# Kernel tuning notes

Measured on AMD Instinct MI355X. Metric: run time of the kernel, lower is better.

## Reference

```python
import jax, jax.numpy as jnp
import numpy as np

B, T, C = 8, 512, 1024
H, E = 16, 64          # n_head, head_dim; H*E == C
L = 2048               # cached (prefix) length in the KV cache


def setup_inputs() -> dict:
    key = jax.random.key(0)
    ks = jax.random.split(key, 6)
    scale = 0.02
    return {
        "x": jax.random.normal(ks[0], (B, T, C), jnp.float32),
        "k_cache": jax.random.normal(ks[1], (B, H, L, E), jnp.float32),
        "v_cache": jax.random.normal(ks[2], (B, H, L, E), jnp.float32),
        "Wqkv": jax.random.normal(ks[3], (C, 3 * C), jnp.float32) * scale,
        "bqkv": jnp.zeros((3 * C,), jnp.float32),
        "Wproj": jax.random.normal(ks[4], (C, C), jnp.float32) * scale,
        "bproj": jnp.zeros((C,), jnp.float32),
    }


def reference(x, k_cache, v_cache, Wqkv, bqkv, Wproj, bproj):
    qkv = x @ Wqkv + bqkv
    q, k, v = jnp.split(qkv, 3, axis=-1)

    def to_heads(t):
        return t.reshape(B, T, H, E).transpose(0, 2, 1, 3)

    q, k, v = to_heads(q), to_heads(k), to_heads(v)

    # append new k,v to the cache (kv_cache.update + get)
    k_full = jnp.concatenate([k_cache, k], axis=2)  # (B,H,L+T,E)
    v_full = jnp.concatenate([v_cache, v], axis=2)

    # manual self-attention with cache-offset causal mask: row i (global pos L+i)
    # may attend to cols j <= L+i  (bias[L:L+T, :L+T])
    att = jnp.einsum("bhte,bhse->bhts", q, k_full) * (1.0 / np.sqrt(E))
    i = jnp.arange(T)[:, None] + L
    j = jnp.arange(L + T)[None, :]
    att = jnp.where(j <= i, att, -jnp.inf)
    att = jax.nn.softmax(att, axis=-1)

    y = jnp.einsum("bhts,bhse->bhte", att, v_full)
    y = y.transpose(0, 2, 1, 3).reshape(B, T, C)
    return y @ Wproj + bproj
```

## Files before the change

### kernel.cpp

```cpp
#include <hip/hip_runtime.h>
#include <hip/hip_bf16.h>

typedef unsigned short u16;
typedef unsigned int u32;

constexpr int B_ = 8, T_ = 512, C_ = 1024, H_ = 16, E_ = 64, L_ = 2048;
constexpr int S_ = L_ + T_;

typedef __bf16 bf16x8 __attribute__((ext_vector_type(8)));
typedef float f32x4 __attribute__((ext_vector_type(4)));
typedef float f32x16 __attribute__((ext_vector_type(16)));

#define QSCALE 0.18033688011112042f


__device__ inline u16 f2bf(float f) {
  u32 u = __float_as_uint(f);
  u32 r = (u + 0x7fffu + ((u >> 16) & 1u)) >> 16;
  return (u16)r;
}

__device__ inline u32 pk2(float a, float b) {
  u32 r;
  asm("v_cvt_pk_bf16_f32 %0, %1, %2" : "=v"(r) : "v"(a), "v"(b));
  return r;
}

__device__ inline void pl32swap(u32& a, u32& b) {
  asm("v_permlane32_swap_b32 %0, %1" : "+v"(a), "+v"(b));
}

__device__ inline void gload_lds16(const u16* g, u16* l) {
  __builtin_amdgcn_global_load_lds(
      (const __attribute__((address_space(1))) u32*)g,
      (__attribute__((address_space(3))) u32*)l, 16, 0, 0);
}

__global__ __launch_bounds__(256) void convert_f32_bf16(const float* __restrict__ in,
                                                        u16* __restrict__ out) {
  const int i = blockIdx.x * 256 + threadIdx.x;
  const float4 a0 = ((const float4*)in)[i * 2];
  const float4 a1 = ((const float4*)in)[i * 2 + 1];
  uint4 p;
  p.x = pk2(a0.x, a0.y);
  p.y = pk2(a0.z, a0.w);
  p.z = pk2(a1.x, a1.y);
  p.w = pk2(a1.z, a1.w);
  ((uint4*)out)[i] = p;
}

__global__ __launch_bounds__(256) void transpose_f32_bf16(const float* __restrict__ in,
                                                          u16* __restrict__ out,
                                                          int R, int Ccols) {
  __shared__ u16 tile[64][65];
  const int r0 = blockIdx.y * 64;
  const int c0 = blockIdx.x * 64;
  const int tr = threadIdx.x >> 6;
  const int tc = threadIdx.x & 63;
#pragma unroll
  for (int i = 0; i < 16; ++i)
    tile[tr + i * 4][tc] = f2bf(in[(size_t)(r0 + tr + i * 4) * Ccols + c0 + tc]);
  __syncthreads();
#pragma unroll
  for (int i = 0; i < 16; ++i)
    out[(size_t)(c0 + tr + i * 4) * R + r0 + tc] = tile[tc][tr + i * 4];
}

__global__ __launch_bounds__(256) void prep_kv(const float* __restrict__ kc,
                                               const float* __restrict__ vc,
                                               u16* __restrict__ Km,
                                               u16* __restrict__ Vtm) {
  __shared__ u16 vt[64 * 72];
  const int s0 = (blockIdx.x & 31) * 64;
  const int bh = blockIdx.x >> 5;
  const int tid = threadIdx.x;
  const int srow = tid >> 2;
  const int eq = (tid & 3) * 16;

  {
    const float* kp = kc + ((size_t)bh * L_ + s0 + srow) * E_ + eq;
    float kv[16];
    *(float4*)(kv + 0) = *(const float4*)(kp + 0);
    *(float4*)(kv + 4) = *(const float4*)(kp + 4);
    *(float4*)(kv + 8) = *(const float4*)(kp + 8);
    *(float4*)(kv + 12) = *(const float4*)(kp + 12);
    uint4 p0, p1;
    p0.x = pk2(kv[0], kv[1]);
    p0.y = pk2(kv[2], kv[3]);
    p0.z = pk2(kv[4], kv[5]);
    p0.w = pk2(kv[6], kv[7]);
    p1.x = pk2(kv[8], kv[9]);
    p1.y = pk2(kv[10], kv[11]);
    p1.z = pk2(kv[12], kv[13]);
    p1.w = pk2(kv[14], kv[15]);
    const int sx = (srow & 7) << 3;
    u16* kd = Km + ((size_t)bh * S_ + s0 + srow) * E_;
    *(uint4*)(kd + (eq ^ sx)) = p0;
    *(uint4*)(kd + ((eq + 8) ^ sx)) = p1;
  }
  {
    const float* vp = vc + ((size_t)bh * L_ + s0 + srow) * E_ + eq;
    float vv[16];
    *(float4*)(vv + 0) = *(const float4*)(vp + 0);
    *(float4*)(vv + 4) = *(const float4*)(vp + 4);
    *(float4*)(vv + 8) = *(const float4*)(vp + 8);
    *(float4*)(vv + 12) = *(const float4*)(vp + 12);
    uint4 p0, p1;
    p0.x = pk2(vv[0], vv[1]);
    p0.y = pk2(vv[2], vv[3]);
    p0.z = pk2(vv[4], vv[5]);
    p0.w = pk2(vv[6], vv[7]);
    p1.x = pk2(vv[8], vv[9]);
    p1.y = pk2(vv[10], vv[11]);
    p1.z = pk2(vv[12], vv[13]);
    p1.w = pk2(vv[14], vv[15]);
    *(uint4*)(vt + srow * 72 + eq) = p0;
    *(uint4*)(vt + srow * 72 + eq + 8) = p1;
  }
  __syncthreads();
  {
    const int erow = tid >> 2;
    const int sq = (tid & 3) * 16;
    u16 o[16];
#pragma unroll
    for (int j = 0; j < 16; ++j) o[j] = vt[(sq + j) * 72 + erow];
    const int ex = (erow & 7) << 3;
    u16* vd = Vtm + ((size_t)bh * E_ + erow) * S_ + s0;
    *(uint4*)(vd + (sq ^ ex)) = *(uint4*)(o + 0);
    *(uint4*)(vd + ((sq + 8) ^ ex)) = *(uint4*)(o + 8);
  }
}

template <int MODE>
__global__ __launch_bounds__(256) void gemm128(const u16* __restrict__ A,
                                               const u16* __restrict__ BT,
                                               const float* __restrict__ bias,
                                               u16* __restrict__ qh,
                                               u16* __restrict__ Km,
                                               u16* __restrict__ Vtm,
                                               float* __restrict__ outf,
                                               int M, int N, int K) {
  __shared__ __align__(16) u16 As[128 * 32];
  __shared__ __align__(16) u16 Bs[128 * 32];
  const int tid = threadIdx.x;
  const int lane = tid & 63;
  const int w = tid >> 6;
  const int m0 = blockIdx.y * 128;
  const int n0 = blockIdx.x * 128;
  const int wm = (w >> 1) * 64;
  const int wn = (w & 1) * 64;
  const int fm = lane & 15;
  const int fk = (lane >> 4) * 8;

  const int srow = w * 16 + (lane >> 2);
  const int scol = (lane & 3) * 8;
  const u16* Ag = A + (size_t)(m0 + srow) * K + scol;
  const u16* Bg = BT + (size_t)(n0 + srow) * K + scol;
  u16* AsU = As + w * 512;
  u16* BsU = Bs + w * 512;

  f32x4 acc[4][4];
#pragma unroll
  for (int i = 0; i < 4; ++i)
#pragma unroll
    for (int j = 0; j < 4; ++j) acc[i][j] = f32x4{0.f, 0.f, 0.f, 0.f};

  for (int k0 = 0; k0 < K; k0 += 32) {
    gload_lds16(Ag, AsU);
    gload_lds16(Ag + (size_t)64 * K, AsU + 2048);
    gload_lds16(Bg, BsU);
    gload_lds16(Bg + (size_t)64 * K, BsU + 2048);
    Ag += 32;
    Bg += 32;
    __syncthreads();
    bf16x8 af[4], bf[4];
#pragma unroll
    for (int i = 0; i < 4; ++i)
      af[i] = *(const bf16x8*)(As + (wm + i * 16 + fm) * 32 + fk);
#pragma unroll
    for (int j = 0; j < 4; ++j)
      bf[j] = *(const bf16x8*)(Bs + (wn + j * 16 + fm) * 32 + fk);
#pragma unroll
    for (int i = 0; i < 4; ++i)
#pragma unroll
      for (int j = 0; j < 4; ++j)
        acc[i][j] = __builtin_amdgcn_mfma_f32_16x16x32_bf16(af[i], bf[j], acc[i][j], 0, 0, 0);
    __syncthreads();
  }

  const int rbase = (lane >> 4) * 4;
  const int cbase = lane & 15;
#pragma unroll
  for (int i = 0; i < 4; ++i)
#pragma unroll
    for (int j = 0; j < 4; ++j) {
      const int n = n0 + wn + j * 16 + cbase;
      const float bv = bias[n];
#pragma unroll
      for (int r = 0; r < 4; ++r) {
        const int m = m0 + wm + i * 16 + rbase + r;
        const float v = acc[i][j][r] + bv;
        if (MODE == 0) {
          const int seg = n >> 10;
          const int c = n & 1023;
          const int e = c & 63;
          const int bhh = ((m >> 9) * H_) + (c >> 6);
          const int t = m & 511;
          if (seg == 0)
            qh[((size_t)bhh * T_ + t) * E_ + e] = f2bf(v * QSCALE);
          else if (seg == 1)
            Km[((size_t)bhh * S_ + L_ + t) * E_ + (e ^ ((t & 7) << 3))] = f2bf(v);
          else
            Vtm[((size_t)bhh * E_ + e) * S_ + ((L_ + t) ^ ((e & 7) << 3))] = f2bf(v);
        } else {
          outf[(size_t)m * N + n] = v;
        }
      }
    }
}

__global__ __launch_bounds__(256) void gemm64(const u16* __restrict__ A,
                                              const u16* __restrict__ BT,
                                              const float* __restrict__ bias,
                                              float* __restrict__ outf,
                                              int M, int N, int K) {
  __shared__ __align__(16) u16 As[64 * 32];
  __shared__ __align__(16) u16 Bs[64 * 32];
  const int tid = threadIdx.x;
  const int lane = tid & 63;
  const int w = tid >> 6;
  const int m0 = blockIdx.y * 64;
  const int n0 = blockIdx.x * 64;
  const int wm = (w >> 1) * 32;
  const int wn = (w & 1) * 32;
  const int fm = lane & 15;
  const int fk = (lane >> 4) * 8;

  const int srow = w * 16 + (lane >> 2);
  const int scol = (lane & 3) * 8;
  const u16* Ag = A + (size_t)(m0 + srow) * K + scol;
  const u16* Bg = BT + (size_t)(n0 + srow) * K + scol;
  u16* AsU = As + w * 512;
  u16* BsU = Bs + w * 512;

  f32x4 acc[2][2];
#pragma unroll
  for (int i = 0; i < 2; ++i)
#pragma unroll
    for (int j = 0; j < 2; ++j) acc[i][j] = f32x4{0.f, 0.f, 0.f, 0.f};

  for (int k0 = 0; k0 < K; k0 += 32) {
    gload_lds16(Ag, AsU);
    gload_lds16(Bg, BsU);
    Ag += 32;
    Bg += 32;
    __syncthreads();
    bf16x8 af[2], bf[2];
#pragma unroll
    for (int i = 0; i < 2; ++i)
      af[i] = *(const bf16x8*)(As + (wm + i * 16 + fm) * 32 + fk);
#pragma unroll
    for (int j = 0; j < 2; ++j)
      bf[j] = *(const bf16x8*)(Bs + (wn + j * 16 + fm) * 32 + fk);
#pragma unroll
    for (int i = 0; i < 2; ++i)
#pragma unroll
      for (int j = 0; j < 2; ++j)
        acc[i][j] = __builtin_amdgcn_mfma_f32_16x16x32_bf16(af[i], bf[j], acc[i][j], 0, 0, 0);
    __syncthreads();
  }

  const int rbase = (lane >> 4) * 4;
  const int cbase = lane & 15;
#pragma unroll
  for (int i = 0; i < 2; ++i)
#pragma unroll
    for (int j = 0; j < 2; ++j) {
      const int n = n0 + wn + j * 16 + cbase;
      const float bv = bias[n];
#pragma unroll
      for (int r = 0; r < 4; ++r) {
        const int m = m0 + wm + i * 16 + rbase + r;
        outf[(size_t)m * N + n] = acc[i][j][r] + bv;
      }
    }
}

__global__ __launch_bounds__(256, 2) void attn_v10(const u16* __restrict__ qh,
                                                   const u16* __restrict__ Km,
                                                   const u16* __restrict__ Vtm,
                                                   u16* __restrict__ y2) {
  __shared__ __align__(16) u16 Ksf[3 * 4096];
  __shared__ __align__(16) u16 Vtsf[3 * 4096];

  const int tid = threadIdx.x;
  const int lane = tid & 63;
  const int w = tid >> 6;
  const int bh = blockIdx.x & 127;
  const int qt = blockIdx.x >> 7;
  const int h = bh & (H_ - 1);
  const int b = bh >> 4;
  const int t0 = qt * 128;

  const int ln = lane & 31;
  const int hi = lane >> 5;
  const int swz = ln & 7;

  const u16* qbase = qh + ((size_t)bh * T_ + t0 + w * 32 + ln) * E_;
  bf16x8 qf[4];
#pragma unroll
  for (int et = 0; et < 4; ++et)
    qf[et] = *(const bf16x8*)(qbase + et * 16 + hi * 8);

  const int l8 = lane >> 3;
  const int u8 = lane & 7;
  const u16* kgl = Km + ((size_t)bh * S_ + w * 16 + l8) * E_ + u8 * 8;
  const u16* vgl = Vtm + ((size_t)bh * E_ + w * 16 + l8) * S_ + u8 * 8;
  const int kdst = w * 1024;

#define STAGE(cc, bi)                                                       \
  do {                                                                      \
    gload_lds16(kgl + (size_t)(cc) * 64 * E_, Ksf + (bi) * 4096 + kdst);    \
    gload_lds16(kgl + ((size_t)(cc) * 64 + 8) * E_,                         \
                Ksf + (bi) * 4096 + kdst + 512);                            \
    gload_lds16(vgl + (cc) * 64, Vtsf + (bi) * 4096 + kdst);                \
    gload_lds16(vgl + (size_t)8 * S_ + (cc) * 64,                           \
                Vtsf + (bi) * 4096 + kdst + 512);                           \
  } while (0)

  f32x16 Yt[2], lacc, zero16;
#pragma unroll
  for (int i = 0; i < 16; ++i) {
    Yt[0][i] = 0.f;
    Yt[1][i] = 0.f;
    lacc[i] = 0.f;
    zero16[i] = 0.f;
  }

  const bf16x8 ones = {(__bf16)1.f, (__bf16)1.f, (__bf16)1.f, (__bf16)1.f,
                       (__bf16)1.f, (__bf16)1.f, (__bf16)1.f, (__bf16)1.f};

  const int qmin_w = L_ + t0 + w * 32;
  const int qpos = qmin_w + ln;
  const int nchunk = (L_ + t0 + 128) >> 6;

#define COMPUTE(cc, BI)                                                        \
  do {                                                                         \
    if (((cc) << 6) <= qmin_w + 31) {                                          \
      const int sbase = (cc) << 6;                                             \
      const u16* ks = Ksf + (BI) * 4096;                                       \
      const u16* vs = Vtsf + (BI) * 4096;                                      \
      bf16x8 pa[4];                                                            \
      _Pragma("unroll") for (int kb = 0; kb < 2; ++kb) {                       \
        f32x16 s;                                                              \
        _Pragma("unroll") for (int et = 0; et < 4; ++et) {                     \
          const bf16x8 kf = *(const bf16x8*)(                                  \
              ks + (kb * 32 + ln) * 64 + (((et * 2 + hi) ^ swz) * 8));         \
          s = __builtin_amdgcn_mfma_f32_32x32x16_bf16(kf, qf[et],              \
                                                      et == 0 ? zero16 : s,    \
                                                      0, 0, 0);                \
        }                                                                      \
        if (sbase + 63 > qmin_w) {                                             \
          const int mb = sbase + kb * 32 + hi * 4;                             \
          _Pragma("unroll") for (int rr = 0; rr < 16; ++rr) {                  \
            const int keypos = mb + (rr & 3) + 8 * (rr >> 2);                  \
            if (keypos > qpos) s[rr] = -1e30f;                                 \
          }                                                                    \
        }                                                                      \
        _Pragma("unroll") for (int rr = 0; rr < 16; ++rr) s[rr] = exp2f(s[rr]);\
        _Pragma("unroll") for (int t = 0; t < 2; ++t) {                        \
          u32 x0 = pk2(s[8 * t + 0], s[8 * t + 1]);                            \
          u32 y0 = pk2(s[8 * t + 4], s[8 * t + 5]);                            \
          u32 x1 = pk2(s[8 * t + 2], s[8 * t + 3]);                            \
          u32 y1 = pk2(s[8 * t + 6], s[8 * t + 7]);                            \
          pl32swap(x0, y0);                                                    \
          pl32swap(x1, y1);                                                    \
          union { u32 u[4]; bf16x8 v; } pu;                                    \
          pu.u[0] = x0;                                                        \
          pu.u[1] = x1;                                                        \
          pu.u[2] = y0;                                                        \
          pu.u[3] = y1;                                                        \
          pa[kb * 2 + t] = pu.v;                                               \
        }                                                                      \
      }                                                                        \
      _Pragma("unroll") for (int t = 0; t < 4; ++t)                            \
        lacc = __builtin_amdgcn_mfma_f32_32x32x16_bf16(ones, pa[t], lacc,      \
                                                       0, 0, 0);               \
      _Pragma("unroll") for (int eb = 0; eb < 2; ++eb)                         \
        _Pragma("unroll") for (int t = 0; t < 4; ++t) {                        \
          const bf16x8 vf = *(const bf16x8*)(                                  \
              vs + (eb * 32 + ln) * 64 + (((t * 2 + hi) ^ swz) * 8));          \
          Yt[eb] = __builtin_amdgcn_mfma_f32_32x32x16_bf16(vf, pa[t], Yt[eb],  \
                                                           0, 0, 0);           \
        }                                                                      \
    }                                                                          \
  } while (0)

#define PHASE(cc, CUR, PF)                                                     \
  do {                                                                         \
    if ((cc) < nchunk) {                                                       \
      if ((cc) + 2 < nchunk) STAGE((cc) + 2, PF);                              \
      COMPUTE((cc), CUR);                                                      \
      if ((cc) + 2 < nchunk)                                                   \
        asm volatile("s_waitcnt vmcnt(4)" ::: "memory");                       \
      else if ((cc) + 1 < nchunk)                                              \
        asm volatile("s_waitcnt vmcnt(0)" ::: "memory");                       \
      if ((cc) + 1 < nchunk) __builtin_amdgcn_s_barrier();                     \
    }                                                                          \
  } while (0)

  STAGE(0, 0);
  STAGE(1, 1);
  asm volatile("s_waitcnt vmcnt(4)" ::: "memory");
  __builtin_amdgcn_s_barrier();

  for (int c = 0; c < nchunk; c += 3) {
    PHASE(c, 0, 2);
    PHASE(c + 1, 1, 0);
    PHASE(c + 2, 2, 1);
  }
#undef PHASE
#undef COMPUTE
#undef STAGE

  const float rl = 1.f / lacc[0];
  const int t_out = t0 + w * 32 + ln;
  u16* yp = y2 + ((size_t)b * T_ + t_out) * C_ + h * E_ + hi * 4;
#pragma unroll
  for (int eb = 0; eb < 2; ++eb)
#pragma unroll
    for (int g = 0; g < 4; ++g) {
      uint2 st;
      st.x = pk2(Yt[eb][4 * g + 0] * rl, Yt[eb][4 * g + 1] * rl);
      st.y = pk2(Yt[eb][4 * g + 2] * rl, Yt[eb][4 * g + 3] * rl);
      *(uint2*)(yp + eb * 32 + g * 8) = st;
    }
}

extern "C" void kernel_launch(void* const* d_in, const int* in_sizes, int n_in,
                              void* d_out, int out_size, void* d_ws, size_t ws_size,
                              hipStream_t stream) {
  const float* x = (const float*)d_in[0];
  const float* kc = (const float*)d_in[1];
  const float* vc = (const float*)d_in[2];
  const float* Wqkv = (const float*)d_in[3];
  const float* bqkv = (const float*)d_in[4];
  const float* Wproj = (const float*)d_in[5];
  const float* bproj = (const float*)d_in[6];
  float* out = (float*)d_out;

  u16* qh = (u16*)d_ws;
  u16* y2 = qh + 4194304;
  u16* xb = y2 + 4194304;
  u16* WqT = xb + 4194304;
  u16* WpT = WqT + 3145728;
  u16* Km = WpT + 1048576;
  u16* Vtm = Km + 20971520;

  convert_f32_bf16<<<dim3(2048), 256, 0, stream>>>(x, xb);
  transpose_f32_bf16<<<dim3(48, 16), 256, 0, stream>>>(Wqkv, WqT, 1024, 3072);
  transpose_f32_bf16<<<dim3(16, 16), 256, 0, stream>>>(Wproj, WpT, 1024, 1024);
  prep_kv<<<dim3(128 * 32), 256, 0, stream>>>(kc, vc, Km, Vtm);

  gemm128<0><<<dim3(24, 32), 256, 0, stream>>>(xb, WqT, bqkv, qh, Km, Vtm, nullptr,
                                               4096, 3072, 1024);

  attn_v10<<<dim3(512), 256, 0, stream>>>(qh, Km, Vtm, y2);

  gemm64<<<dim3(16, 64), 256, 0, stream>>>(y2, WpT, bproj, out, 4096, 1024, 1024);
}
```

Measured before the change: 326.3 us.

## Use raw exp2, vectorize V epilogue stores, and enlarge output-projection GEMM tile

In the attention kernel, exp2f is replaced by the hardware v_exp_f32 instruction (builtin or inline asm) to drop range-handling overhead. The QKV GEMM epilogue is restructured so the transposed V writes are packed into 8-byte stores of four bf16 values instead of four scalar stores. The output projection GEMM moves from 64x64 tiles to 128x64 tiles, so each wave computes 4x2 MFMA fragments, which improves reuse of the B operand. Larger tiles halve the grid to 512 blocks, and the raw exp2 drops denormal handling, which is harmless here because the inputs are mostly negative.

Result: faster. 313.7 us (-3.8%).

```diff
diff --git a/kernel.cpp b/kernel.cpp
--- a/kernel.cpp
+++ b/kernel.cpp
@@ -29,6 +29,20 @@
 __device__ inline void pl32swap(u32& a, u32& b) {
   asm("v_permlane32_swap_b32 %0, %1" : "+v"(a), "+v"(b));
 }
+
+#if defined(__has_builtin)
+#if __has_builtin(__builtin_amdgcn_exp2f)
+#define EXP2(x) __builtin_amdgcn_exp2f(x)
+#endif
+#endif
+#ifndef EXP2
+__device__ inline float exp2_raw_(float x) {
+  float r;
+  asm("v_exp_f32 %0, %1" : "=v"(r) : "v"(x));
+  return r;
+}
+#define EXP2(x) exp2_raw_(x)
+#endif
 
 __device__ inline void gload_lds16(const u16* g, u16* l) {
   __builtin_amdgcn_global_load_lds(
@@ -191,47 +205,58 @@
   const int rbase = (lane >> 4) * 4;
   const int cbase = lane & 15;
 #pragma unroll
-  for (int i = 0; i < 4; ++i)
+  for (int i = 0; i < 4; ++i) {
+    const int mb = m0 + wm + i * 16 + rbase;
+    const int t = mb & 511;
+    const int bq = mb >> 9;
 #pragma unroll
     for (int j = 0; j < 4; ++j) {
       const int n = n0 + wn + j * 16 + cbase;
       const float bv = bias[n];
-#pragma unroll
-      for (int r = 0; r < 4; ++r) {
-        const int m = m0 + wm + i * 16 + rbase + r;
-        const float v = acc[i][j][r] + bv;
-        if (MODE == 0) {
-          const int seg = n >> 10;
-          const int c = n & 1023;
-          const int e = c & 63;
-          const int bhh = ((m >> 9) * H_) + (c >> 6);
-          const int t = m & 511;
-          if (seg == 0)
-            qh[((size_t)bhh * T_ + t) * E_ + e] = f2bf(v * QSCALE);
-          else if (seg == 1)
-            Km[((size_t)bhh * S_ + L_ + t) * E_ + (e ^ ((t & 7) << 3))] = f2bf(v);
-          else
-            Vtm[((size_t)bhh * E_ + e) * S_ + ((L_ + t) ^ ((e & 7) << 3))] = f2bf(v);
+      if (MODE == 0) {
+        const int seg = n >> 10;
+        const int c = n & 1023;
+        const int e = c & 63;
+        const int bhh = bq * H_ + (c >> 6);
+        if (seg == 0) {
+#pragma unroll
+          for (int r = 0; r < 4; ++r)
+            qh[((size_t)bhh * T_ + t + r) * E_ + e] =
+                f2bf((acc[i][j][r] + bv) * QSCALE);
+        } else if (seg == 1) {
+#pragma unroll
+          for (int r = 0; r < 4; ++r)
+            Km[((size_t)bhh * S_ + L_ + t + r) * E_ + (e ^ (((t + r) & 7) << 3))] =
+                f2bf(acc[i][j][r] + bv);
         } else {
-          outf[(size_t)m * N + n] = v;
+          uint2 pv;
+          pv.x = pk2(acc[i][j][0] + bv, acc[i][j][1] + bv);
+          pv.y = pk2(acc[i][j][2] + bv, acc[i][j][3] + bv);
+          *(uint2*)(Vtm + ((size_t)bhh * E_ + e) * S_ +
+                    ((L_ + t) ^ ((e & 7) << 3))) = pv;
         }
+      } else {
+#pragma unroll
+        for (int r = 0; r < 4; ++r)
+          outf[(size_t)(mb + r) * N + n] = acc[i][j][r] + bv;
       }
     }
-}
-
-__global__ __launch_bounds__(256) void gemm64(const u16* __restrict__ A,
-                                              const u16* __restrict__ BT,
-                                              const float* __restrict__ bias,
-                                              float* __restrict__ outf,
-                                              int M, int N, int K) {
-  __shared__ __align__(16) u16 As[64 * 32];
+  }
+}
+
+__global__ __launch_bounds__(256) void gemm12864(const u16* __restrict__ A,
+                                                 const u16* __restrict__ BT,
+                                                 const float* __restrict__ bias,
+                                                 float* __restrict__ outf,
+                                                 int M, int N, int K) {
+  __shared__ __align__(16) u16 As[128 * 32];
   __shared__ __align__(16) u16 Bs[64 * 32];
   const int tid = threadIdx.x;
   const int lane = tid & 63;
   const int w = tid >> 6;
-  const int m0 = blockIdx.y * 64;
+  const int m0 = blockIdx.y * 128;
   const int n0 = blockIdx.x * 64;
-  const int wm = (w >> 1) * 32;
+  const int wm = (w >> 1) * 64;
   const int wn = (w & 1) * 32;
   const int fm = lane & 15;
   const int fk = (lane >> 4) * 8;
@@ -243,27 +268,28 @@
   u16* AsU = As + w * 512;
   u16* BsU = Bs + w * 512;
 
-  f32x4 acc[2][2];
-#pragma unroll
-  for (int i = 0; i < 2; ++i)
+  f32x4 acc[4][2];
+#pragma unroll
+  for (int i = 0; i < 4; ++i)
 #pragma unroll
     for (int j = 0; j < 2; ++j) acc[i][j] = f32x4{0.f, 0.f, 0.f, 0.f};
 
   for (int k0 = 0; k0 < K; k0 += 32) {
     gload_lds16(Ag, AsU);
+    gload_lds16(Ag + (size_t)64 * K, AsU + 2048);
     gload_lds16(Bg, BsU);
     Ag += 32;
     Bg += 32;
     __syncthreads();
-    bf16x8 af[2], bf[2];
-#pragma unroll
-    for (int i = 0; i < 2; ++i)
+    bf16x8 af[4], bf[2];
+#pragma unroll
+    for (int i = 0; i < 4; ++i)
       af[i] = *(const bf16x8*)(As + (wm + i * 16 + fm) * 32 + fk);
 #pragma unroll
     for (int j = 0; j < 2; ++j)
       bf[j] = *(const bf16x8*)(Bs + (wn + j * 16 + fm) * 32 + fk);
 #pragma unroll
-    for (int i = 0; i < 2; ++i)
+    for (int i = 0; i < 4; ++i)
 #pragma unroll
       for (int j = 0; j < 2; ++j)
         acc[i][j] = __builtin_amdgcn_mfma_f32_16x16x32_bf16(af[i], bf[j], acc[i][j], 0, 0, 0);
@@ -273,7 +299,7 @@
   const int rbase = (lane >> 4) * 4;
   const int cbase = lane & 15;
 #pragma unroll
-  for (int i = 0; i < 2; ++i)
+  for (int i = 0; i < 4; ++i)
 #pragma unroll
     for (int j = 0; j < 2; ++j) {
       const int n = n0 + wn + j * 16 + cbase;
@@ -286,7 +312,7 @@
     }
 }
 
-__global__ __launch_bounds__(256, 2) void attn_v10(const u16* __restrict__ qh,
+__global__ __launch_bounds__(256, 2) void attn_v11(const u16* __restrict__ qh,
                                                    const u16* __restrict__ Km,
                                                    const u16* __restrict__ Vtm,
                                                    u16* __restrict__ y2) {
@@ -367,7 +393,7 @@
             if (keypos > qpos) s[rr] = -1e30f;                                 \
           }                                                                    \
         }                                                                      \
-        _Pragma("unroll") for (int rr = 0; rr < 16; ++rr) s[rr] = exp2f(s[rr]);\
+        _Pragma("unroll") for (int rr = 0; rr < 16; ++rr) s[rr] = EXP2(s[rr]); \
         _Pragma("unroll") for (int t = 0; t < 2; ++t) {                        \
           u32 x0 = pk2(s[8 * t + 0], s[8 * t + 1]);                            \
           u32 y0 = pk2(s[8 * t + 4], s[8 * t + 5]);                            \
@@ -465,7 +491,7 @@
   gemm128<0><<<dim3(24, 32), 256, 0, stream>>>(xb, WqT, bqkv, qh, Km, Vtm, nullptr,
                                                4096, 3072, 1024);
 
-  attn_v10<<<dim3(512), 256, 0, stream>>>(qh, Km, Vtm, y2);
-
-  gemm64<<<dim3(16, 64), 256, 0, stream>>>(y2, WpT, bproj, out, 4096, 1024, 1024);
-}
+  attn_v11<<<dim3(512), 256, 0, stream>>>(qh, Km, Vtm, y2);
+
+  gemm12864<<<dim3(16, 32), 256, 0, stream>>>(y2, WpT, bproj, out, 4096, 1024, 1024);
+}
```
